# Performance work log

Measured on AMD Instinct MI355X. Metric: run time of the kernel, lower is better.

The kernel has to match this reference:

```python
import jax, jax.numpy as jnp
import numpy as np

B, L, H, NH, DH = 2, 4096, 768, 12, 64
W_ = 128          # one-sided sliding window
NL = 2            # encoder layers
VOCAB, OUT, FF = 50265, 384, 3072
EPS = 1e-5


def _ln(x, s, b):
    m = jnp.mean(x, axis=-1, keepdims=True)
    v = jnp.mean((x - m) ** 2, axis=-1, keepdims=True)
    return (x - m) / jnp.sqrt(v + EPS) * s + b


def _attn(x, amask, Wq, bq, Wk, bk, Wv, bv, Wo, bo):
    # x: [B,L,H]; sliding-window attention (one-sided W_) + global token 0
    def heads(Wt, bt):
        return (x @ Wt + bt).reshape(B, L, NH, DH).transpose(0, 2, 1, 3)  # [B,NH,L,DH]
    q, k, v = heads(Wq, bq), heads(Wk, bk), heads(Wv, bv)
    scale = 1.0 / np.sqrt(DH).astype(np.float32)
    C = W_
    nC = L // C
    qc = q.reshape(B, NH, nC, C, DH)

    def blocks(t):  # gather [prev, self, next] key chunks -> [B,NH,nC,3C,DH]
        tc = t.reshape(B, NH, nC, C, DH)
        tp = jnp.pad(tc, ((0, 0), (0, 0), (1, 1), (0, 0), (0, 0)))
        return jnp.concatenate([tp[:, :, :-2], tp[:, :, 1:-1], tp[:, :, 2:]], axis=3)

    k3, v3 = blocks(k), blocks(v)
    s_loc = jnp.einsum('bhncd,bhnkd->bhnck', qc, k3) * scale  # [B,NH,nC,C,3C]

    pos_k = (jnp.arange(nC)[:, None] - 1) * C + jnp.arange(3 * C)[None, :]  # [nC,3C]
    pos_q = jnp.arange(nC)[:, None] * C + jnp.arange(C)[None, :]            # [nC,C]
    within = jnp.abs(pos_q[:, :, None] - pos_k[:, None, :]) <= W_           # [nC,C,3C]
    valid = (pos_k >= 0) & (pos_k < L) & (pos_k != 0)  # key 0 handled as global column
    mk = amask[:, jnp.clip(pos_k, 0, L - 1)] > 0        # [B,nC,3C]
    m = within[None, None] & valid[None, None, :, None, :] & mk[:, None, :, None, :]
    s_loc = jnp.where(m, s_loc, -1e9)

    # every token also attends to the global token 0
    s_g = jnp.einsum('bhld,bhd->bhl', q, k[:, :, 0]) * scale  # [B,NH,L]
    s = jnp.concatenate([s_loc.reshape(B, NH, L, 3 * C), s_g[..., None]], axis=-1)
    p = jax.nn.softmax(s, axis=-1)
    p_loc = p[..., :3 * C].reshape(B, NH, nC, C, 3 * C)
    out = jnp.einsum('bhnck,bhnkd->bhncd', p_loc, v3).reshape(B, NH, L, DH)
    out = out + p[..., -1:] * v[:, :, 0][:, :, None, :]

    # global token 0 attends to everything
    s0 = jnp.einsum('bhd,bhld->bhl', q[:, :, 0], k) * scale
    s0 = jnp.where(amask[:, None, :] > 0, s0, -1e9)
    o0 = jnp.einsum('bhl,bhld->bhd', jax.nn.softmax(s0, axis=-1), v)
    out = out.at[:, :, 0, :].set(o0)

    out = out.transpose(0, 2, 1, 3).reshape(B, L, H)
    return out @ Wo + bo


def setup_inputs() -> dict:
    key = jax.random.key(0)
    ks = jax.random.split(key, 16)
    p = lambda k_, sh: 0.02 * jax.random.normal(k_, sh, jnp.float32)
    return {
        'input_ids': jax.random.randint(ks[0], (B, L), 0, VOCAB, dtype=jnp.int32),
        'attention_mask': jnp.ones((B, L), jnp.int32),
        'word_emb': p(ks[1], (VOCAB, H)),
        'pos_emb': p(ks[2], (L, H)),
        'emb_ln_s': jnp.ones((H,), jnp.float32), 'emb_ln_b': jnp.zeros((H,), jnp.float32),
        'Wq': p(ks[3], (NL, H, H)), 'bq': jnp.zeros((NL, H), jnp.float32),
        'Wk': p(ks[4], (NL, H, H)), 'bk': jnp.zeros((NL, H), jnp.float32),
        'Wv': p(ks[5], (NL, H, H)), 'bv': jnp.zeros((NL, H), jnp.float32),
        'Wo': p(ks[6], (NL, H, H)), 'bo': jnp.zeros((NL, H), jnp.float32),
        'ln1_s': jnp.ones((NL, H), jnp.float32), 'ln1_b': jnp.zeros((NL, H), jnp.float32),
        'W1': p(ks[7], (NL, H, FF)), 'b1': jnp.zeros((NL, FF), jnp.float32),
        'W2': p(ks[8], (NL, FF, H)), 'b2': jnp.zeros((NL, H), jnp.float32),
        'ln2_s': jnp.ones((NL, H), jnp.float32), 'ln2_b': jnp.zeros((NL, H), jnp.float32),
        'Wfc': p(ks[9], (H, OUT)), 'bfc': jnp.zeros((OUT,), jnp.float32),
    }


def reference(input_ids, attention_mask, word_emb, pos_emb, emb_ln_s, emb_ln_b,
              Wq, bq, Wk, bk, Wv, bv, Wo, bo, ln1_s, ln1_b,
              W1, b1, W2, b2, ln2_s, ln2_b, Wfc, bfc):
    x = word_emb[input_ids] + pos_emb[None]
    x = _ln(x, emb_ln_s, emb_ln_b)
    for l in range(NL):
        a = _attn(x, attention_mask, Wq[l], bq[l], Wk[l], bk[l], Wv[l], bv[l], Wo[l], bo[l])
        x = _ln(x + a, ln1_s[l], ln1_b[l])
        h = jax.nn.gelu(x @ W1[l] + b1[l])
        x = _ln(x + h @ W2[l] + b2[l], ln2_s[l], ln2_b[l])
    v_dn = x @ Wfc + bfc           # [B,L,OUT]
    cls = v_dn[:, 0]               # fc(last_hidden[:,0]) == v_dn[:,0]
    return v_dn, cls
```

## Files before the change

kernel.cpp:

```cpp
#include <hip/hip_runtime.h>
#include <hip/hip_bf16.h>
#include <stdint.h>

#define L_SEQ 4096
#define H_DIM 768
#define N_HEADS 12
#define D_HEAD 64
#define N_CHUNK 32
#define CHUNK 128
#define FF_DIM 3072
#define OUT_DIM 384
#define BATCH 2
#define EPS_LN 1e-5f
#define M_ROWS (BATCH * L_SEQ)
#define QKV_LD (3 * H_DIM)
#define NSEG 16

typedef unsigned short u16;
typedef __bf16 bx8 __attribute__((ext_vector_type(8)));
typedef float fx4 __attribute__((ext_vector_type(4)));
typedef u16 ux8 __attribute__((ext_vector_type(8)));

__device__ __forceinline__ u16 f2bf(float f) {
  union { float f; unsigned u; } x; x.f = f;
  unsigned r = x.u + 0x7fffu + ((x.u >> 16) & 1u);
  return (u16)(r >> 16);
}
__device__ __forceinline__ float bf2f(u16 v) {
  union { unsigned u; float f; } x; x.u = ((unsigned)v) << 16;
  return x.f;
}

__device__ __forceinline__ void gload16(const void* g, void* l) {
  __builtin_amdgcn_global_load_lds((const __attribute__((address_space(1))) void*)g,
                                   (__attribute__((address_space(3))) void*)l, 16, 0, 0);
}

template<int OUT_BF16, int DO_GELU>
__global__ __launch_bounds__(256, 3)
void gemm_s(const u16* __restrict__ A, const u16* __restrict__ Bt,
            const float* __restrict__ bias,
            float* __restrict__ Cf, u16* __restrict__ Cb,
            int N, int K)
{
  __shared__ __align__(16) u16 As[128 * 64];
  __shared__ __align__(16) u16 Bs[128 * 64];
  const int tid = threadIdx.x;
  const int lane = tid & 63, w = tid >> 6;
  const int c16 = lane & 15, g = lane >> 4;
  const int wr = w >> 1, wc = w & 1;

  const int nbn = N >> 7;
  int id = blockIdx.x;
  id = (id & 7) * (gridDim.x >> 3) + (id >> 3);
  const int bm = id / nbn, bn = id % nbn;

  const int srow = w * 8 + (lane >> 3);
  const int schunk = (lane & 7) ^ (lane >> 3);
  const u16* sA = A + (size_t)(bm * 128 + srow) * K + schunk * 8;
  const u16* sB = Bt + (size_t)(bn * 128 + srow) * K + schunk * 8;
  const int wdst = w * 512;

  fx4 acc[4][4] = {};

  for (int k0 = 0; k0 < K; k0 += 64) {
    #pragma unroll
    for (int i = 0; i < 4; i++) {
      gload16(sA + (size_t)(i * 32) * K + k0, &As[i * 2048 + wdst]);
      gload16(sB + (size_t)(i * 32) * K + k0, &Bs[i * 2048 + wdst]);
    }
    __syncthreads();
    #pragma unroll
    for (int h = 0; h < 2; h++) {
      bx8 af[4], bf[4];
      #pragma unroll
      for (int m = 0; m < 4; m++) {
        const int row = wr * 64 + m * 16 + c16;
        af[m] = *(const bx8*)&As[row * 64 + (((h << 2) + g) ^ (c16 & 7)) * 8];
      }
      #pragma unroll
      for (int n = 0; n < 4; n++) {
        const int row = wc * 64 + n * 16 + c16;
        bf[n] = *(const bx8*)&Bs[row * 64 + (((h << 2) + g) ^ (c16 & 7)) * 8];
      }
      #pragma unroll
      for (int m = 0; m < 4; m++)
        #pragma unroll
        for (int n = 0; n < 4; n++)
          acc[m][n] = __builtin_amdgcn_mfma_f32_16x16x32_bf16(af[m], bf[n], acc[m][n], 0, 0, 0);
    }
    __syncthreads();
  }

  const int row0 = bm * 128 + wr * 64 + g * 4;
  const int col0 = bn * 128 + wc * 64 + c16;
  #pragma unroll
  for (int n = 0; n < 4; n++) {
    const int col = col0 + n * 16;
    const float bb = bias[col];
    #pragma unroll
    for (int m = 0; m < 4; m++) {
      #pragma unroll
      for (int r = 0; r < 4; r++) {
        float y = acc[m][n][r] + bb;
        if (DO_GELU) {
          const float tt = y;
          y = 0.5f * tt * (1.0f + tanhf(0.7978845608f * (tt + 0.044715f * tt * tt * tt)));
        }
        const size_t idx = (size_t)(row0 + m * 16 + r) * N + col;
        if (OUT_BF16) Cb[idx] = f2bf(y);
        else Cf[idx] = y;
      }
    }
  }
}

#define V_STR 424

__global__ __launch_bounds__(512, 2)
void attn_local_kernel(const u16* __restrict__ qkv, const int* __restrict__ amask,
                       u16* __restrict__ attnout)
{
  __shared__ __align__(16) u16 Vlds[64 * V_STR];
  __shared__ __align__(16) u16 Plds[8 * 16 * V_STR];

  const int tid = threadIdx.x;
  const int lane = tid & 63, w = tid >> 6;
  const int c16 = lane & 15, g = lane >> 4;

  const int bh = blockIdx.x >> 5;
  const int n = blockIdx.x & 31;
  const int b = bh / N_HEADS, h = bh % N_HEADS;

  const u16* qkvb = qkv + (size_t)b * L_SEQ * QKV_LD + h * D_HEAD;
  const int chunk_lo = n * CHUNK - CHUNK;

  for (int idx = tid; idx < 416 * 8; idx += 512) {
    const int j = idx >> 3, d8 = (idx & 7) * 8;
    if (j >= 385) {
      #pragma unroll
      for (int i = 0; i < 8; i++) Vlds[(d8 + i) * V_STR + j] = 0;
    } else {
      int pos = (j == 384) ? 0 : chunk_lo + j;
      if (pos < 0 || pos >= L_SEQ) pos = 0;
      ux8 vv = *(const ux8*)(qkvb + (size_t)pos * QKV_LD + 2 * H_DIM + d8);
      #pragma unroll
      for (int i = 0; i < 8; i++) Vlds[(d8 + i) * V_STR + j] = vv[i];
    }
  }

  const int qrow = n * CHUNK + w * 16 + c16;
  const u16* qp = qkvb + (size_t)qrow * QKV_LD + g * 8;
  const bx8 aq0 = *(const bx8*)qp;
  const bx8 aq1 = *(const bx8*)(qp + 32);

  unsigned kvm = 0;
  #pragma unroll
  for (int kf = 0; kf < 24; kf++) {
    const int pos = chunk_lo + kf * 16 + c16;
    bool ok = (pos >= 1) && (pos < L_SEQ);
    if (ok) ok = (amask[b * L_SEQ + pos] > 0);
    kvm |= ((unsigned)ok) << kf;
  }

  fx4 s[26];
  #pragma unroll
  for (int kf = 0; kf < 25; kf++) {
    int pos = (kf == 24) ? 0 : chunk_lo + kf * 16 + c16;
    if (pos < 0 || pos >= L_SEQ) pos = 0;
    const u16* kp = qkvb + (size_t)pos * QKV_LD + H_DIM + g * 8;
    const bx8 b0 = *(const bx8*)kp;
    const bx8 b1 = *(const bx8*)(kp + 32);
    fx4 a = {};
    a = __builtin_amdgcn_mfma_f32_16x16x32_bf16(aq0, b0, a, 0, 0, 0);
    a = __builtin_amdgcn_mfma_f32_16x16x32_bf16(aq1, b1, a, 0, 0, 0);
    s[kf] = a;
  }

  const int cq = w * 16 + g * 4;
  float mx[4], sm[4];
  #pragma unroll
  for (int r = 0; r < 4; r++) mx[r] = -3.0e38f;
  #pragma unroll
  for (int kf = 0; kf < 25; kf++) {
    const int j = kf * 16 + c16;
    const bool kv = (kf < 24) ? (((kvm >> kf) & 1u) != 0) : (c16 == 0);
    #pragma unroll
    for (int r = 0; r < 4; r++) {
      const int c = cq + r;
      const bool keep = kv && (kf == 24 || (j >= c && j <= c + 256));
      const float val = keep ? s[kf][r] * 0.125f : -1.0e9f;
      s[kf][r] = val;
      mx[r] = fmaxf(mx[r], val);
    }
  }
  #pragma unroll
  for (int r = 0; r < 4; r++) {
    float m = mx[r];
    m = fmaxf(m, __shfl_xor(m, 1));
    m = fmaxf(m, __shfl_xor(m, 2));
    m = fmaxf(m, __shfl_xor(m, 4));
    m = fmaxf(m, __shfl_xor(m, 8));
    mx[r] = m;
    sm[r] = 0.f;
  }
  #pragma unroll
  for (int kf = 0; kf < 25; kf++)
    #pragma unroll
    for (int r = 0; r < 4; r++) {
      const float p = __expf(s[kf][r] - mx[r]);
      s[kf][r] = p;
      sm[r] += p;
    }
  float rinv[4];
  #pragma unroll
  for (int r = 0; r < 4; r++) {
    float t = sm[r];
    t += __shfl_xor(t, 1);
    t += __shfl_xor(t, 2);
    t += __shfl_xor(t, 4);
    t += __shfl_xor(t, 8);
    rinv[r] = 1.0f / t;
  }
  s[25] = (fx4){0.f, 0.f, 0.f, 0.f};

  u16* pb = Plds + (size_t)w * 16 * V_STR;
  #pragma unroll
  for (int kf = 0; kf < 26; kf++) {
    const int j = kf * 16 + c16;
    #pragma unroll
    for (int r = 0; r < 4; r++)
      pb[(g * 4 + r) * V_STR + j] = f2bf(s[kf][r]);
  }
  __syncthreads();

  fx4 o[4] = {};
  const u16* pr = Plds + (size_t)(w * 16 + c16) * V_STR + g * 8;
  #pragma unroll
  for (int kt = 0; kt < 13; kt++) {
    const bx8 pa = *(const bx8*)(pr + kt * 32);
    #pragma unroll
    for (int df = 0; df < 4; df++) {
      const bx8 vvf = *(const bx8*)&Vlds[(df * 16 + c16) * V_STR + kt * 32 + g * 8];
      o[df] = __builtin_amdgcn_mfma_f32_16x16x32_bf16(pa, vvf, o[df], 0, 0, 0);
    }
  }

  u16* ob = attnout + (size_t)b * L_SEQ * H_DIM + h * D_HEAD;
  const int posq = n * CHUNK + w * 16 + g * 4;
  #pragma unroll
  for (int df = 0; df < 4; df++)
    #pragma unroll
    for (int r = 0; r < 4; r++)
      ob[(size_t)(posq + r) * H_DIM + df * 16 + c16] = f2bf(o[df][r] * rinv[r]);
}

__global__ __launch_bounds__(256)
void attn_g_score(const u16* __restrict__ qkv, const int* __restrict__ amask,
                  float* __restrict__ sbuf, float* __restrict__ pmax)
{
  __shared__ float qs[D_HEAD];
  __shared__ float red[4];
  const int seg = blockIdx.x, bh = blockIdx.y;
  const int b = bh / N_HEADS, h = bh % N_HEADS;
  const u16* base = qkv + (size_t)b * L_SEQ * QKV_LD + h * D_HEAD;
  const int tid = threadIdx.x;

  if (tid < D_HEAD) qs[tid] = bf2f(base[tid]);
  __syncthreads();

  const int l = seg * 256 + tid;
  const ux8* kp = (const ux8*)(base + (size_t)l * QKV_LD + H_DIM);
  float dot = 0.f;
  #pragma unroll
  for (int i = 0; i < 8; i++) {
    const ux8 kv = kp[i];
    #pragma unroll
    for (int j = 0; j < 8; j++) dot += qs[i * 8 + j] * bf2f(kv[j]);
  }
  float sv = dot * 0.125f;
  if (amask[b * L_SEQ + l] == 0) sv = -1.0e9f;
  sbuf[(size_t)bh * L_SEQ + l] = sv;

  float m = sv;
  #pragma unroll
  for (int off = 32; off > 0; off >>= 1) m = fmaxf(m, __shfl_xor(m, off));
  if ((tid & 63) == 0) red[tid >> 6] = m;
  __syncthreads();
  if (tid == 0)
    pmax[bh * NSEG + seg] = fmaxf(fmaxf(red[0], red[1]), fmaxf(red[2], red[3]));
}

__global__ __launch_bounds__(256)
void attn_g_pv(const u16* __restrict__ qkv, const float* __restrict__ sbuf,
               const float* __restrict__ pmax, float* __restrict__ psum,
               float* __restrict__ po)
{
  __shared__ float es[256];
  __shared__ float red[4];
  const int seg = blockIdx.x, bh = blockIdx.y;
  const int b = bh / N_HEADS, h = bh % N_HEADS;
  const int tid = threadIdx.x;

  float M = -3.0e38f;
  #pragma unroll
  for (int i = 0; i < NSEG; i++) M = fmaxf(M, pmax[bh * NSEG + i]);

  const int l = seg * 256 + tid;
  const float e = __expf(sbuf[(size_t)bh * L_SEQ + l] - M);
  es[tid] = e;

  float t = e;
  #pragma unroll
  for (int off = 32; off > 0; off >>= 1) t += __shfl_xor(t, off);
  if ((tid & 63) == 0) red[tid >> 6] = t;
  __syncthreads();
  if (tid == 0) psum[bh * NSEG + seg] = red[0] + red[1] + red[2] + red[3];

  const int d = tid & 63, grp = tid >> 6;
  const u16* vb = qkv + (size_t)b * L_SEQ * QKV_LD + h * D_HEAD + 2 * H_DIM + d;
  float acc = 0.f;
  #pragma unroll 4
  for (int i = 0; i < 64; i++) {
    const int ll = seg * 256 + grp * 64 + i;
    acc += es[grp * 64 + i] * bf2f(vb[(size_t)ll * QKV_LD]);
  }
  po[(((size_t)bh * NSEG + seg) * 4 + grp) * D_HEAD + d] = acc;
}

__global__ __launch_bounds__(64)
void attn_g_combine(const float* __restrict__ psum, const float* __restrict__ po,
                    u16* __restrict__ attnout)
{
  const int bh = blockIdx.x;
  const int b = bh / N_HEADS, h = bh % N_HEADS;
  const int d = threadIdx.x;
  float S = 0.f;
  #pragma unroll
  for (int i = 0; i < NSEG; i++) S += psum[bh * NSEG + i];
  float acc = 0.f;
  #pragma unroll
  for (int i = 0; i < NSEG * 4; i++)
    acc += po[((size_t)bh * NSEG * 4 + i) * D_HEAD + d];
  attnout[(size_t)b * L_SEQ * H_DIM + h * D_HEAD + d] = f2bf(acc / S);
}

__device__ __forceinline__ void block_stats(float sum, float sq, float* red,
                                            float& mean, float& rstd)
{
  const int lane = threadIdx.x & 63, wv = threadIdx.x >> 6;
  #pragma unroll
  for (int off = 32; off > 0; off >>= 1) {
    sum += __shfl_xor(sum, off);
    sq  += __shfl_xor(sq, off);
  }
  if (lane == 0) { red[wv] = sum; red[4 + wv] = sq; }
  __syncthreads();
  sum = red[0] + red[1] + red[2] + red[3];
  sq  = red[4] + red[5] + red[6] + red[7];
  mean = sum * (1.0f / H_DIM);
  const float var = sq * (1.0f / H_DIM) - mean * mean;
  rstd = rsqrtf(var + EPS_LN);
}

__global__ __launch_bounds__(256)
void embed_ln_kernel(const int* __restrict__ ids, const float* __restrict__ wemb,
                     const float* __restrict__ pemb, const float* __restrict__ gam,
                     const float* __restrict__ bet, float* __restrict__ xf,
                     u16* __restrict__ xb)
{
  __shared__ float red[8];
  const int row = blockIdx.x, tid = threadIdx.x;
  const int l = row & (L_SEQ - 1);
  const int id = ids[row];
  float v[3]; float sum = 0.f, sq = 0.f;
  #pragma unroll
  for (int i = 0; i < 3; i++) {
    const int c = tid + i * 256;
    const float t = wemb[(size_t)id * H_DIM + c] + pemb[(size_t)l * H_DIM + c];
    v[i] = t; sum += t; sq += t * t;
  }
  float mean, rstd;
  block_stats(sum, sq, red, mean, rstd);
  #pragma unroll
  for (int i = 0; i < 3; i++) {
    const int c = tid + i * 256;
    const float y = (v[i] - mean) * rstd * gam[c] + bet[c];
    xf[(size_t)row * H_DIM + c] = y;
    xb[(size_t)row * H_DIM + c] = f2bf(y);
  }
}

__global__ __launch_bounds__(256)
void add_ln_kernel(float* xio, const float* __restrict__ yin,
                   const float* __restrict__ gam, const float* __restrict__ bet,
                   u16* __restrict__ xb)
{
  __shared__ float red[8];
  const int row = blockIdx.x, tid = threadIdx.x;
  float v[3]; float sum = 0.f, sq = 0.f;
  #pragma unroll
  for (int i = 0; i < 3; i++) {
    const int c = tid + i * 256;
    const float t = xio[(size_t)row * H_DIM + c] + yin[(size_t)row * H_DIM + c];
    v[i] = t; sum += t; sq += t * t;
  }
  float mean, rstd;
  block_stats(sum, sq, red, mean, rstd);
  #pragma unroll
  for (int i = 0; i < 3; i++) {
    const int c = tid + i * 256;
    const float y = (v[i] - mean) * rstd * gam[c] + bet[c];
    xio[(size_t)row * H_DIM + c] = y;
    xb[(size_t)row * H_DIM + c] = f2bf(y);
  }
}

__global__ __launch_bounds__(256)
void transpose_w_kernel(const float* __restrict__ W, u16* __restrict__ Wt, int K, int N)
{
  __shared__ float tile[32][33];
  const int k0 = blockIdx.x * 32, n0 = blockIdx.y * 32;
  const int tx = threadIdx.x & 31, ty = threadIdx.x >> 5;
  #pragma unroll
  for (int i = 0; i < 32; i += 8)
    tile[ty + i][tx] = W[(size_t)(k0 + ty + i) * N + n0 + tx];
  __syncthreads();
  #pragma unroll
  for (int i = 0; i < 32; i += 8)
    Wt[(size_t)(n0 + ty + i) * K + k0 + tx] = f2bf(tile[tx][ty + i]);
}

__global__ void concat3_kernel(const float* __restrict__ a, const float* __restrict__ b,
                               const float* __restrict__ c, float* __restrict__ out)
{
  const int i = blockIdx.x * 256 + threadIdx.x;
  if (i < H_DIM) out[i] = a[i];
  else if (i < 2 * H_DIM) out[i] = b[i - H_DIM];
  else if (i < 3 * H_DIM) out[i] = c[i - 2 * H_DIM];
}

__global__ void cls_copy_kernel(const float* __restrict__ vdn, float* __restrict__ cls)
{
  const int i = blockIdx.x * 256 + threadIdx.x;
  if (i < BATCH * OUT_DIM)
    cls[i] = vdn[(size_t)(i / OUT_DIM) * L_SEQ * OUT_DIM + (i % OUT_DIM)];
}

extern "C" void kernel_launch(void* const* d_in, const int* in_sizes, int n_in,
                              void* d_out, int out_size, void* d_ws, size_t ws_size,
                              hipStream_t stream)
{
  (void)in_sizes; (void)n_in; (void)out_size; (void)ws_size;
  const int*   ids   = (const int*)d_in[0];
  const int*   amask = (const int*)d_in[1];
  const float* wemb  = (const float*)d_in[2];
  const float* pemb  = (const float*)d_in[3];
  const float* elns  = (const float*)d_in[4];
  const float* elnb  = (const float*)d_in[5];
  const float* Wq    = (const float*)d_in[6];
  const float* bq    = (const float*)d_in[7];
  const float* Wk    = (const float*)d_in[8];
  const float* bk    = (const float*)d_in[9];
  const float* Wv    = (const float*)d_in[10];
  const float* bv    = (const float*)d_in[11];
  const float* Wo    = (const float*)d_in[12];
  const float* bo    = (const float*)d_in[13];
  const float* ln1s  = (const float*)d_in[14];
  const float* ln1b  = (const float*)d_in[15];
  const float* W1    = (const float*)d_in[16];
  const float* b1    = (const float*)d_in[17];
  const float* W2    = (const float*)d_in[18];
  const float* b2    = (const float*)d_in[19];
  const float* ln2s  = (const float*)d_in[20];
  const float* ln2b  = (const float*)d_in[21];
  const float* Wfc   = (const float*)d_in[22];
  const float* bfc   = (const float*)d_in[23];

  char* ws = (char*)d_ws;
  size_t off = 0;
  auto alloc = [&](size_t bytes) -> void* {
    void* p = ws + off;
    off += (bytes + 255) & ~(size_t)255;
    return p;
  };
  float* xf   = (float*)alloc((size_t)M_ROWS * H_DIM * 4);
  float* proj = (float*)alloc((size_t)M_ROWS * H_DIM * 4);
  u16* xb     = (u16*)alloc((size_t)M_ROWS * H_DIM * 2);
  u16* big    = (u16*)alloc((size_t)M_ROWS * FF_DIM * 2);
  u16* attno  = (u16*)alloc((size_t)M_ROWS * H_DIM * 2);
  u16* wqkvT  = (u16*)alloc((size_t)QKV_LD * H_DIM * 2);
  u16* woT    = (u16*)alloc((size_t)H_DIM * H_DIM * 2);
  u16* w1T    = (u16*)alloc((size_t)FF_DIM * H_DIM * 2);
  u16* w2T    = (u16*)alloc((size_t)H_DIM * FF_DIM * 2);
  u16* wfcT   = (u16*)alloc((size_t)OUT_DIM * H_DIM * 2);
  float* bqkv = (float*)alloc(QKV_LD * 4);
  float* gsc  = (float*)alloc((size_t)BATCH * N_HEADS * L_SEQ * 4);
  float* gpm  = (float*)alloc((size_t)BATCH * N_HEADS * NSEG * 4);
  float* gps  = (float*)alloc((size_t)BATCH * N_HEADS * NSEG * 4);
  float* gpo  = (float*)alloc((size_t)BATCH * N_HEADS * NSEG * 4 * D_HEAD * 4);

  u16* qkvb = big;
  u16* ff1  = big;

  embed_ln_kernel<<<M_ROWS, 256, 0, stream>>>(ids, wemb, pemb, elns, elnb, xf, xb);

  for (int l = 0; l < 2; l++) {
    const size_t wof = (size_t)l * H_DIM * H_DIM;
    transpose_w_kernel<<<dim3(24, 24), 256, 0, stream>>>(Wq + wof, wqkvT, H_DIM, H_DIM);
    transpose_w_kernel<<<dim3(24, 24), 256, 0, stream>>>(Wk + wof, wqkvT + (size_t)H_DIM * H_DIM, H_DIM, H_DIM);
    transpose_w_kernel<<<dim3(24, 24), 256, 0, stream>>>(Wv + wof, wqkvT + (size_t)2 * H_DIM * H_DIM, H_DIM, H_DIM);
    transpose_w_kernel<<<dim3(24, 24), 256, 0, stream>>>(Wo + wof, woT, H_DIM, H_DIM);
    transpose_w_kernel<<<dim3(24, 96), 256, 0, stream>>>(W1 + (size_t)l * H_DIM * FF_DIM, w1T, H_DIM, FF_DIM);
    transpose_w_kernel<<<dim3(96, 24), 256, 0, stream>>>(W2 + (size_t)l * FF_DIM * H_DIM, w2T, FF_DIM, H_DIM);
    concat3_kernel<<<9, 256, 0, stream>>>(bq + l * H_DIM, bk + l * H_DIM, bv + l * H_DIM, bqkv);

    gemm_s<1, 0><<<(M_ROWS / 128) * (QKV_LD / 128), 256, 0, stream>>>(
        xb, wqkvT, bqkv, nullptr, qkvb, QKV_LD, H_DIM);
    attn_local_kernel<<<BATCH * N_HEADS * N_CHUNK, 512, 0, stream>>>(qkvb, amask, attno);
    attn_g_score<<<dim3(NSEG, BATCH * N_HEADS), 256, 0, stream>>>(qkvb, amask, gsc, gpm);
    attn_g_pv<<<dim3(NSEG, BATCH * N_HEADS), 256, 0, stream>>>(qkvb, gsc, gpm, gps, gpo);
    attn_g_combine<<<BATCH * N_HEADS, 64, 0, stream>>>(gps, gpo, attno);
    gemm_s<0, 0><<<(M_ROWS / 128) * (H_DIM / 128), 256, 0, stream>>>(
        attno, woT, bo + l * H_DIM, proj, nullptr, H_DIM, H_DIM);
    add_ln_kernel<<<M_ROWS, 256, 0, stream>>>(xf, proj, ln1s + l * H_DIM, ln1b + l * H_DIM, xb);
    gemm_s<1, 1><<<(M_ROWS / 128) * (FF_DIM / 128), 256, 0, stream>>>(
        xb, w1T, b1 + l * FF_DIM, nullptr, ff1, FF_DIM, H_DIM);
    gemm_s<0, 0><<<(M_ROWS / 128) * (H_DIM / 128), 256, 0, stream>>>(
        ff1, w2T, b2 + l * H_DIM, proj, nullptr, H_DIM, FF_DIM);
    add_ln_kernel<<<M_ROWS, 256, 0, stream>>>(xf, proj, ln2s + l * H_DIM, ln2b + l * H_DIM, xb);
  }

  transpose_w_kernel<<<dim3(24, 12), 256, 0, stream>>>(Wfc, wfcT, H_DIM, OUT_DIM);
  float* vdn = (float*)d_out;
  gemm_s<0, 0><<<(M_ROWS / 128) * (OUT_DIM / 128), 256, 0, stream>>>(
      xb, wfcT, bfc, vdn, nullptr, OUT_DIM, H_DIM);
  cls_copy_kernel<<<3, 256, 0, stream>>>(vdn, vdn + (size_t)BATCH * L_SEQ * OUT_DIM);
}
```

Before: 675.1 us.

## Store residual stream in bf16, batch weight prep, fuse cls copy

The fp32 residual buffer and fp32 projection outputs are dropped. The residual is kept only in bf16, and the Wo and W2 GEMMs write bf16, which roughly halves the traffic into and out of the add+LayerNorm kernels. All per-layer weight transposes and bias concatenations are merged into a single launch at the start, and the cls copy is folded into the final GEMM epilogue, cutting launch count. The trade is precision: the residual stream is now rounded to bf16 at each layer, which may raise numerical error.

```diff
diff --git a/kernel.cpp b/kernel.cpp
--- a/kernel.cpp
+++ b/kernel.cpp
@@ -36,11 +36,12 @@
                                    (__attribute__((address_space(3))) void*)l, 16, 0, 0);
 }
 
-template<int OUT_BF16, int DO_GELU>
+template<int OUT_BF16, int DO_GELU, int DO_CLS>
 __global__ __launch_bounds__(256, 3)
 void gemm_s(const u16* __restrict__ A, const u16* __restrict__ Bt,
             const float* __restrict__ bias,
             float* __restrict__ Cf, u16* __restrict__ Cb,
+            float* __restrict__ cls,
             int N, int K)
 {
   __shared__ __align__(16) u16 As[128 * 64];
@@ -107,9 +108,14 @@
           const float tt = y;
           y = 0.5f * tt * (1.0f + tanhf(0.7978845608f * (tt + 0.044715f * tt * tt * tt)));
         }
-        const size_t idx = (size_t)(row0 + m * 16 + r) * N + col;
+        const int row = row0 + m * 16 + r;
+        const size_t idx = (size_t)row * N + col;
         if (OUT_BF16) Cb[idx] = f2bf(y);
         else Cf[idx] = y;
+        if (DO_CLS) {
+          if ((row & (L_SEQ - 1)) == 0)
+            cls[(row >> 12) * OUT_DIM + col] = y;
+        }
       }
     }
   }
@@ -366,8 +372,7 @@
 __global__ __launch_bounds__(256)
 void embed_ln_kernel(const int* __restrict__ ids, const float* __restrict__ wemb,
                      const float* __restrict__ pemb, const float* __restrict__ gam,
-                     const float* __restrict__ bet, float* __restrict__ xf,
-                     u16* __restrict__ xb)
+                     const float* __restrict__ bet, u16* __restrict__ xb)
 {
   __shared__ float red[8];
   const int row = blockIdx.x, tid = threadIdx.x;
@@ -386,15 +391,13 @@
   for (int i = 0; i < 3; i++) {
     const int c = tid + i * 256;
     const float y = (v[i] - mean) * rstd * gam[c] + bet[c];
-    xf[(size_t)row * H_DIM + c] = y;
     xb[(size_t)row * H_DIM + c] = f2bf(y);
   }
 }
 
 __global__ __launch_bounds__(256)
-void add_ln_kernel(float* xio, const float* __restrict__ yin,
-                   const float* __restrict__ gam, const float* __restrict__ bet,
-                   u16* __restrict__ xb)
+void add_ln_kernel(u16* xio, const u16* __restrict__ yin,
+                   const float* __restrict__ gam, const float* __restrict__ bet)
 {
   __shared__ float red[8];
   const int row = blockIdx.x, tid = threadIdx.x;
@@ -402,7 +405,7 @@
   #pragma unroll
   for (int i = 0; i < 3; i++) {
     const int c = tid + i * 256;
-    const float t = xio[(size_t)row * H_DIM + c] + yin[(size_t)row * H_DIM + c];
+    const float t = bf2f(xio[(size_t)row * H_DIM + c]) + bf2f(yin[(size_t)row * H_DIM + c]);
     v[i] = t; sum += t; sq += t * t;
   }
   float mean, rstd;
@@ -411,40 +414,66 @@
   for (int i = 0; i < 3; i++) {
     const int c = tid + i * 256;
     const float y = (v[i] - mean) * rstd * gam[c] + bet[c];
-    xio[(size_t)row * H_DIM + c] = y;
-    xb[(size_t)row * H_DIM + c] = f2bf(y);
+    xio[(size_t)row * H_DIM + c] = f2bf(y);
   }
 }
 
 __global__ __launch_bounds__(256)
-void transpose_w_kernel(const float* __restrict__ W, u16* __restrict__ Wt, int K, int N)
-{
+void prep_weights(const float* __restrict__ Wq, const float* __restrict__ Wk,
+                  const float* __restrict__ Wv, const float* __restrict__ Wo,
+                  const float* __restrict__ W1, const float* __restrict__ W2,
+                  const float* __restrict__ Wfc,
+                  const float* __restrict__ bq, const float* __restrict__ bk,
+                  const float* __restrict__ bv,
+                  u16* __restrict__ wqkvT, u16* __restrict__ woT,
+                  u16* __restrict__ w1T, u16* __restrict__ w2T,
+                  u16* __restrict__ wfcT, float* __restrict__ bqkv)
+{
+  const int t = blockIdx.x;
+  const int tid = threadIdx.x;
+  if (t >= 14112) {
+    const int idx = t - 14112;
+    const int l = idx / 9, j = idx % 9;
+    const int i = j * 256 + tid;
+    if (i < H_DIM)          bqkv[l * QKV_LD + i] = bq[l * H_DIM + i];
+    else if (i < 2 * H_DIM) bqkv[l * QKV_LD + i] = bk[l * H_DIM + i - H_DIM];
+    else if (i < 3 * H_DIM) bqkv[l * QKV_LD + i] = bv[l * H_DIM + i - 2 * H_DIM];
+    return;
+  }
+  const float* src; u16* dst; int K, N, r;
+  if (t < 13824) {
+    const int l = t / 6912; r = t % 6912;
+    if (r < 2304) {
+      const int m = r / 576; r = r % 576; K = H_DIM; N = H_DIM;
+      if (m == 0)      src = Wq + (size_t)l * H_DIM * H_DIM;
+      else if (m == 1) src = Wk + (size_t)l * H_DIM * H_DIM;
+      else if (m == 2) src = Wv + (size_t)l * H_DIM * H_DIM;
+      else             src = Wo + (size_t)l * H_DIM * H_DIM;
+      dst = (m < 3) ? wqkvT + (size_t)l * QKV_LD * H_DIM + (size_t)m * H_DIM * H_DIM
+                    : woT + (size_t)l * H_DIM * H_DIM;
+    } else if (r < 4608) {
+      r -= 2304; K = H_DIM; N = FF_DIM;
+      src = W1 + (size_t)l * H_DIM * FF_DIM;
+      dst = w1T + (size_t)l * FF_DIM * H_DIM;
+    } else {
+      r -= 4608; K = FF_DIM; N = H_DIM;
+      src = W2 + (size_t)l * FF_DIM * H_DIM;
+      dst = w2T + (size_t)l * H_DIM * FF_DIM;
+    }
+  } else {
+    r = t - 13824; K = H_DIM; N = OUT_DIM; src = Wfc; dst = wfcT;
+  }
+  const int ntn = N >> 5;
+  const int k0 = (r / ntn) * 32, n0 = (r % ntn) * 32;
   __shared__ float tile[32][33];
-  const int k0 = blockIdx.x * 32, n0 = blockIdx.y * 32;
-  const int tx = threadIdx.x & 31, ty = threadIdx.x >> 5;
+  const int tx = tid & 31, ty = tid >> 5;
   #pragma unroll
   for (int i = 0; i < 32; i += 8)
-    tile[ty + i][tx] = W[(size_t)(k0 + ty + i) * N + n0 + tx];
+    tile[ty + i][tx] = src[(size_t)(k0 + ty + i) * N + n0 + tx];
   __syncthreads();
   #pragma unroll
   for (int i = 0; i < 32; i += 8)
-    Wt[(size_t)(n0 + ty + i) * K + k0 + tx] = f2bf(tile[tx][ty + i]);
-}
-
-__global__ void concat3_kernel(const float* __restrict__ a, const float* __restrict__ b,
-                               const float* __restrict__ c, float* __restrict__ out)
-{
-  const int i = blockIdx.x * 256 + threadIdx.x;
-  if (i < H_DIM) out[i] = a[i];
-  else if (i < 2 * H_DIM) out[i] = b[i - H_DIM];
-  else if (i < 3 * H_DIM) out[i] = c[i - 2 * H_DIM];
-}
-
-__global__ void cls_copy_kernel(const float* __restrict__ vdn, float* __restrict__ cls)
-{
-  const int i = blockIdx.x * 256 + threadIdx.x;
-  if (i < BATCH * OUT_DIM)
-    cls[i] = vdn[(size_t)(i / OUT_DIM) * L_SEQ * OUT_DIM + (i % OUT_DIM)];
+    dst[(size_t)(n0 + ty + i) * K + k0 + tx] = f2bf(tile[tx][ty + i]);
 }
 
 extern "C" void kernel_launch(void* const* d_in, const int* in_sizes, int n_in,
@@ -484,17 +513,16 @@
     off += (bytes + 255) & ~(size_t)255;
     return p;
   };
-  float* xf   = (float*)alloc((size_t)M_ROWS * H_DIM * 4);
-  float* proj = (float*)alloc((size_t)M_ROWS * H_DIM * 4);
   u16* xb     = (u16*)alloc((size_t)M_ROWS * H_DIM * 2);
+  u16* projb  = (u16*)alloc((size_t)M_ROWS * H_DIM * 2);
   u16* big    = (u16*)alloc((size_t)M_ROWS * FF_DIM * 2);
   u16* attno  = (u16*)alloc((size_t)M_ROWS * H_DIM * 2);
-  u16* wqkvT  = (u16*)alloc((size_t)QKV_LD * H_DIM * 2);
-  u16* woT    = (u16*)alloc((size_t)H_DIM * H_DIM * 2);
-  u16* w1T    = (u16*)alloc((size_t)FF_DIM * H_DIM * 2);
-  u16* w2T    = (u16*)alloc((size_t)H_DIM * FF_DIM * 2);
+  u16* wqkvT  = (u16*)alloc((size_t)2 * QKV_LD * H_DIM * 2);
+  u16* woT    = (u16*)alloc((size_t)2 * H_DIM * H_DIM * 2);
+  u16* w1T    = (u16*)alloc((size_t)2 * FF_DIM * H_DIM * 2);
+  u16* w2T    = (u16*)alloc((size_t)2 * H_DIM * FF_DIM * 2);
   u16* wfcT   = (u16*)alloc((size_t)OUT_DIM * H_DIM * 2);
-  float* bqkv = (float*)alloc(QKV_LD * 4);
+  float* bqkv = (float*)alloc(2 * QKV_LD * 4);
   float* gsc  = (float*)alloc((size_t)BATCH * N_HEADS * L_SEQ * 4);
   float* gpm  = (float*)alloc((size_t)BATCH * N_HEADS * NSEG * 4);
   float* gps  = (float*)alloc((size_t)BATCH * N_HEADS * NSEG * 4);
@@ -503,37 +531,34 @@
   u16* qkvb = big;
   u16* ff1  = big;
 
-  embed_ln_kernel<<<M_ROWS, 256, 0, stream>>>(ids, wemb, pemb, elns, elnb, xf, xb);
+  prep_weights<<<14130, 256, 0, stream>>>(Wq, Wk, Wv, Wo, W1, W2, Wfc,
+                                          bq, bk, bv,
+                                          wqkvT, woT, w1T, w2T, wfcT, bqkv);
+  embed_ln_kernel<<<M_ROWS, 256, 0, stream>>>(ids, wemb, pemb, elns, elnb, xb);
 
   for (int l = 0; l < 2; l++) {
-    const size_t wof = (size_t)l * H_DIM * H_DIM;
-    transpose_w_kernel<<<dim3(24, 24), 256, 0, stream>>>(Wq + wof, wqkvT, H_DIM, H_DIM);
-    transpose_w_kernel<<<dim3(24, 24), 256, 0, stream>>>(Wk + wof, wqkvT + (size_t)H_DIM * H_DIM, H_DIM, H_DIM);
-    transpose_w_kernel<<<dim3(24, 24), 256, 0, stream>>>(Wv + wof, wqkvT + (size_t)2 * H_DIM * H_DIM, H_DIM, H_DIM);
-    transpose_w_kernel<<<dim3(24, 24), 256, 0, stream>>>(Wo + wof, woT, H_DIM, H_DIM);
-    transpose_w_kernel<<<dim3(24, 96), 256, 0, stream>>>(W1 + (size_t)l * H_DIM * FF_DIM, w1T, H_DIM, FF_DIM);
-    transpose_w_kernel<<<dim3(96, 24), 256, 0, stream>>>(W2 + (size_t)l * FF_DIM * H_DIM, w2T, FF_DIM, H_DIM);
-    concat3_kernel<<<9, 256, 0, stream>>>(bq + l * H_DIM, bk + l * H_DIM, bv + l * H_DIM, bqkv);
-
-    gemm_s<1, 0><<<(M_ROWS / 128) * (QKV_LD / 128), 256, 0, stream>>>(
-        xb, wqkvT, bqkv, nullptr, qkvb, QKV_LD, H_DIM);
+    gemm_s<1, 0, 0><<<(M_ROWS / 128) * (QKV_LD / 128), 256, 0, stream>>>(
+        xb, wqkvT + (size_t)l * QKV_LD * H_DIM, bqkv + l * QKV_LD,
+        nullptr, qkvb, nullptr, QKV_LD, H_DIM);
     attn_local_kernel<<<BATCH * N_HEADS * N_CHUNK, 512, 0, stream>>>(qkvb, amask, attno);
     attn_g_score<<<dim3(NSEG, BATCH * N_HEADS), 256, 0, stream>>>(qkvb, amask, gsc, gpm);
     attn_g_pv<<<dim3(NSEG, BATCH * N_HEADS), 256, 0, stream>>>(qkvb, gsc, gpm, gps, gpo);
     attn_g_combine<<<BATCH * N_HEADS, 64, 0, stream>>>(gps, gpo, attno);
-    gemm_s<0, 0><<<(M_ROWS / 128) * (H_DIM / 128), 256, 0, stream>>>(
-        attno, woT, bo + l * H_DIM, proj, nullptr, H_DIM, H_DIM);
-    add_ln_kernel<<<M_ROWS, 256, 0, stream>>>(xf, proj, ln1s + l * H_DIM, ln1b + l * H_DIM, xb);
-    gemm_s<1, 1><<<(M_ROWS / 128) * (FF_DIM / 128), 256, 0, stream>>>(
-        xb, w1T, b1 + l * FF_DIM, nullptr, ff1, FF_DIM, H_DIM);
-    gemm_s<0, 0><<<(M_ROWS / 128) * (H_DIM / 128), 256, 0, stream>>>(
-        ff1, w2T, b2 + l * H_DIM, proj, nullptr, H_DIM, FF_DIM);
-    add_ln_kernel<<<M_ROWS, 256, 0, stream>>>(xf, proj, ln2s + l * H_DIM, ln2b + l * H_DIM, xb);
-  }
-
-  transpose_w_kernel<<<dim3(24, 12), 256, 0, stream>>>(Wfc, wfcT, H_DIM, OUT_DIM);
+    gemm_s<1, 0, 0><<<(M_ROWS / 128) * (H_DIM / 128), 256, 0, stream>>>(
+        attno, woT + (size_t)l * H_DIM * H_DIM, bo + l * H_DIM,
+        nullptr, projb, nullptr, H_DIM, H_DIM);
+    add_ln_kernel<<<M_ROWS, 256, 0, stream>>>(xb, projb, ln1s + l * H_DIM, ln1b + l * H_DIM);
+    gemm_s<1, 1, 0><<<(M_ROWS / 128) * (FF_DIM / 128), 256, 0, stream>>>(
+        xb, w1T + (size_t)l * FF_DIM * H_DIM, b1 + l * FF_DIM,
+        nullptr, ff1, nullptr, FF_DIM, H_DIM);
+    gemm_s<1, 0, 0><<<(M_ROWS / 128) * (H_DIM / 128), 256, 0, stream>>>(
+        ff1, w2T + (size_t)l * H_DIM * FF_DIM, b2 + l * H_DIM,
+        nullptr, projb, nullptr, H_DIM, FF_DIM);
+    add_ln_kernel<<<M_ROWS, 256, 0, stream>>>(xb, projb, ln2s + l * H_DIM, ln2b + l * H_DIM);
+  }
+
   float* vdn = (float*)d_out;
-  gemm_s<0, 0><<<(M_ROWS / 128) * (OUT_DIM / 128), 256, 0, stream>>>(
-      xb, wfcT, bfc, vdn, nullptr, OUT_DIM, H_DIM);
-  cls_copy_kernel<<<3, 256, 0, stream>>>(vdn, vdn + (size_t)BATCH * L_SEQ * OUT_DIM);
-}
+  float* cls = vdn + (size_t)BATCH * L_SEQ * OUT_DIM;
+  gemm_s<0, 0, 1><<<(M_ROWS / 128) * (OUT_DIM / 128), 256, 0, stream>>>(
+      xb, wfcT, bfc, vdn, nullptr, cls, OUT_DIM, H_DIM);
+}
```

Result: faster. 616.0 us (-8.8%).
